# Kernel optimization log

Hardware: AMD Instinct MI355X
Metric: run time of the kernel (lower is better)

Reference implementation:

```python
import jax, jax.numpy as jnp
import numpy as np

N = 8192
E = 262144
NODE_IN = 128
EDGE_IN = 64
OUT = 128


def setup_inputs() -> dict:
    key = jax.random.key(0)
    k1, k2, k3, k4, k5 = jax.random.split(key, 5)
    x = jax.random.normal(k1, (N, NODE_IN), dtype=jnp.float32)
    edge_index = jax.random.randint(k2, (2, E), 0, N, dtype=jnp.int64)
    edge_attr = jax.random.normal(k3, (E, EDGE_IN), dtype=jnp.float32)
    W = jax.random.normal(k4, (OUT, NODE_IN), dtype=jnp.float32) / np.sqrt(NODE_IN)
    a = jax.random.normal(k5, (1, 2 * OUT + EDGE_IN), dtype=jnp.float32) / np.sqrt(2 * OUT + EDGE_IN)
    return {"x": x, "edge_index": edge_index, "edge_attr": edge_attr, "W": W, "a": a}


def reference(x, edge_index, edge_attr, W, a):
    # h = W(x): [N, out]
    h = x @ W.T
    src, dst = edge_index[0], edge_index[1]
    # per-edge concat [h_src, h_dst, edge_attr]: [E, 2*out + edge_in]
    a_input = jnp.concatenate([h[src], h[dst], edge_attr], axis=1)
    # e = leakyrelu(a(a_input)): [E]
    e = jax.nn.leaky_relu(a_input @ a.T, negative_slope=0.2).squeeze(-1)
    n = h.shape[0]
    # dense scatter into NxN (non-edges stay 0 and DO participate in softmax,
    # matching the original torch module)
    attention = jnp.zeros((n, n), dtype=x.dtype).at[src, dst].set(e)
    attention = jax.nn.softmax(attention, axis=1)
    # aggregate: [N, out]
    return attention @ h
```

## Files before the change

### kernel.cpp

```cpp
#include <hip/hip_runtime.h>

#define N_NODES 8192
#define N_EDGES 262144
#define CAP 128
#define BM 16
#define NB_GEMM 512
#define NEB2 1024
#define NSB 32

typedef float vf4 __attribute__((ext_vector_type(4)));

__device__ inline unsigned short f2bf(float f) {
    unsigned u = __float_as_uint(f);
    u += 0x7FFF + ((u >> 16) & 1);
    return (unsigned short)(u >> 16);
}

__global__ __launch_bounds__(256) void k_gemm(const float* __restrict__ x,
                                              const float* __restrict__ W,
                                              const float* __restrict__ a,
                                              unsigned short* __restrict__ h2,
                                              float* __restrict__ asrc,
                                              float* __restrict__ adst,
                                              float* __restrict__ Spart,
                                              int* __restrict__ counts) {
    __shared__ float wlds[128 * 128];
    __shared__ float xlds[BM * 128];
    __shared__ float csum_l[4 * 130];

    const int tid = threadIdx.x;
    const int tc = tid & 63;
    const int tr = tid >> 6;
    const int r0 = blockIdx.x * BM;

    if (tid < BM) counts[blockIdx.x * BM + tid] = 0;

    #pragma unroll
    for (int i = tid; i < BM * 32; i += 256) {
        const int row = i >> 5, k4 = (i & 31) << 2;
        const vf4 v = __builtin_nontemporal_load(
            reinterpret_cast<const vf4*>(&x[(size_t)(r0 + row) * 128 + k4]));
        *reinterpret_cast<vf4*>(&xlds[row * 128 + k4]) = v;
    }
    #pragma unroll
    for (int i = tid; i < 4096; i += 256) {
        const int wr = i >> 5, k4 = (i & 31) << 2;
        const int ks = k4 ^ (((wr >> 1) & 31) << 2);
        *reinterpret_cast<float4*>(&wlds[wr * 128 + ks]) =
            *reinterpret_cast<const float4*>(&W[(size_t)wr * 128 + k4]);
    }
    __syncthreads();

    float acc[4][2] = {};
    const int R0 = 2 * tc;
    const int sw = (tc & 31) << 2;
    #pragma unroll 8
    for (int k0 = 0; k0 < 128; k0 += 4) {
        const int ks = k0 ^ sw;
        const float4 w0 = *reinterpret_cast<const float4*>(&wlds[R0 * 128 + ks]);
        const float4 w1 = *reinterpret_cast<const float4*>(&wlds[(R0 + 1) * 128 + ks]);
        #pragma unroll
        for (int r = 0; r < 4; ++r) {
            const float4 xv = *reinterpret_cast<const float4*>(&xlds[(4 * tr + r) * 128 + k0]);
            acc[r][0] += xv.x*w0.x + xv.y*w0.y + xv.z*w0.z + xv.w*w0.w;
            acc[r][1] += xv.x*w1.x + xv.y*w1.y + xv.z*w1.z + xv.w*w1.w;
        }
    }

    #pragma unroll
    for (int r = 0; r < 4; ++r) {
        ushort2 o; o.x = f2bf(acc[r][0]); o.y = f2bf(acc[r][1]);
        *reinterpret_cast<ushort2*>(&h2[(size_t)(r0 + 4 * tr + r) * 128 + 2 * tc]) = o;
    }
    {
        float2 cs;
        cs.x = acc[0][0] + acc[1][0] + acc[2][0] + acc[3][0];
        cs.y = acc[0][1] + acc[1][1] + acc[2][1] + acc[3][1];
        *reinterpret_cast<float2*>(&csum_l[tr * 130 + 2 * tc]) = cs;
    }

    const float a10 = a[2*tc], a11 = a[2*tc+1];
    const float a20 = a[128+2*tc], a21 = a[128+2*tc+1];
    #pragma unroll
    for (int r = 0; r < 4; ++r) {
        float v1 = acc[r][0]*a10 + acc[r][1]*a11;
        float v2 = acc[r][0]*a20 + acc[r][1]*a21;
        #pragma unroll
        for (int o = 32; o > 0; o >>= 1) { v1 += __shfl_down(v1, o); v2 += __shfl_down(v2, o); }
        if (tc == 0) { asrc[r0 + 4*tr + r] = v1; adst[r0 + 4*tr + r] = v2; }
    }
    __syncthreads();
    if (tid < 128) {
        const float s = csum_l[tid] + csum_l[130 + tid] + csum_l[260 + tid] + csum_l[390 + tid];
        Spart[(size_t)blockIdx.x * 128 + tid] = s;
    }
}

__global__ __launch_bounds__(256) void k_edge(const int* __restrict__ ei,
                                              const float* __restrict__ ea,
                                              const float* __restrict__ a,
                                              const float* __restrict__ asrc,
                                              const float* __restrict__ adst,
                                              int* __restrict__ counts,
                                              int2* __restrict__ bucket,
                                              const float* __restrict__ Spart,
                                              float* __restrict__ S) {
    const int blk = blockIdx.x;
    const int tid = threadIdx.x;
    if (blk >= NEB2) {
        const int c = (blk - NEB2) * 4 + (tid >> 6);
        const int l = tid & 63;
        float s = 0.f;
        #pragma unroll
        for (int j = 0; j < 8; ++j) s += Spart[(size_t)(l + 64 * j) * 128 + c];
        #pragma unroll
        for (int o = 32; o > 0; o >>= 1) s += __shfl_down(s, o);
        if (l == 0) S[c] = s;
        return;
    }
    __shared__ float d_l[256];
    const int lane16 = tid & 15;
    const int grp = tid >> 4;
    const int ebase = blk * 256;
    const int eid = ebase + tid;

    const int s = __builtin_nontemporal_load(&ei[eid]);
    const int t = __builtin_nontemporal_load(&ei[N_EDGES + eid]);
    const float as_ = asrc[s];
    const float at_ = adst[t];

    const float4 av = *reinterpret_cast<const float4*>(&a[256 + lane16 * 4]);
    #pragma unroll 4
    for (int p = 0; p < 16; ++p) {
        const int e2 = ebase + p * 16 + grp;
        const vf4 ev = __builtin_nontemporal_load(
            reinterpret_cast<const vf4*>(&ea[(size_t)e2 * 64 + lane16 * 4]));
        float d = ev.x*av.x + ev.y*av.y + ev.z*av.z + ev.w*av.w;
        d += __shfl_xor(d, 1);
        d += __shfl_xor(d, 2);
        d += __shfl_xor(d, 4);
        d += __shfl_xor(d, 8);
        if (lane16 == 0) d_l[p * 16 + grp] = d;
    }
    __syncthreads();
    const float v = as_ + at_ + d_l[tid];
    const float ev = v > 0.f ? v : 0.2f * v;
    const int pos = atomicAdd(&counts[s], 1);
    if (pos < CAP) {
        int2 rec;
        rec.x = (int)(((unsigned)eid << 13) | (unsigned)t);
        rec.y = __float_as_int(ev);
        bucket[(size_t)s * CAP + pos] = rec;
    }
}

__global__ __launch_bounds__(256) void k_row(const int2* __restrict__ bucket2,
                                             const int* __restrict__ counts,
                                             const unsigned short* __restrict__ h2,
                                             const float* __restrict__ S,
                                             float* __restrict__ out) {
    __shared__ __align__(16) int key_l[2][CAP];
    __shared__ float e_l[2][CAP];
    __shared__ float cw[2][CAP];
    __shared__ int cd[2][CAP];
    __shared__ float redm[2][2], reds[2][2];
    __shared__ float4 xw[2][32];
    __shared__ int nw_s[2];

    const int tid = threadIdx.x;
    const int sub = tid >> 7;
    const int t = tid & 127;
    const int q = t & 31;
    const int g = t >> 5;
    const int row = blockIdx.x * 2 + sub;
    const float4 Sv4 = *reinterpret_cast<const float4*>(&S[4 * q]);

    const int2 rec = bucket2[(size_t)row * CAP + t];
    int k = counts[row];
    if (k > CAP) k = CAP;
    const int kpad = (k + 3) & ~3;
    if (t < k) {
        key_l[sub][t] = rec.x;
        e_l[sub][t] = __int_as_float(rec.y);
    } else if (t < kpad) {
        key_l[sub][t] = -1;
    }
    if (t == 0) nw_s[sub] = 0;
    __syncthreads();

    float mloc = 0.f;
    if (t < k) {
        const int key = key_l[sub][t];
        bool win = true;
        for (int s2 = 0; s2 < kpad; s2 += 4) {
            const int4 kv = *reinterpret_cast<const int4*>(&key_l[sub][s2]);
            const bool hit = (((kv.x ^ key) & 8191) == 0 && kv.x > key)
                          || (((kv.y ^ key) & 8191) == 0 && kv.y > key)
                          || (((kv.z ^ key) & 8191) == 0 && kv.z > key)
                          || (((kv.w ^ key) & 8191) == 0 && kv.w > key);
            win = win && !hit;
        }
        if (win) {
            const float ev = e_l[sub][t];
            mloc = ev > 0.f ? ev : 0.f;
            const int p = atomicAdd(&nw_s[sub], 1);
            cd[sub][p] = key & 8191;
            cw[sub][p] = ev;
        }
    }
    #pragma unroll
    for (int o = 32; o > 0; o >>= 1) mloc = fmaxf(mloc, __shfl_down(mloc, o));
    if ((t & 63) == 0) redm[sub][t >> 6] = mloc;
    __syncthreads();
    const float m = fmaxf(redm[sub][0], redm[sub][1]);
    const int nw = nw_s[sub];
    const float w0 = expf(-m);
    float sloc = 0.f;
    if (t < nw) {
        const float w = expf(cw[sub][t] - m);
        sloc = w;
        cw[sub][t] = w - w0;
    }
    #pragma unroll
    for (int o = 32; o > 0; o >>= 1) sloc += __shfl_down(sloc, o);
    if ((t & 63) == 0) reds[sub][t >> 6] = sloc;
    __syncthreads();
    const float D = (float)(N_NODES - nw) * w0 + reds[sub][0] + reds[sub][1];

    float4 acc0 = {0.f, 0.f, 0.f, 0.f}, acc1 = {0.f, 0.f, 0.f, 0.f};
    int j = g;
    for (; j + 4 < nw; j += 8) {
        const float c0 = cw[sub][j], c1 = cw[sub][j + 4];
        const int d0 = cd[sub][j], d1 = cd[sub][j + 4];
        const ushort4 u0 = *reinterpret_cast<const ushort4*>(&h2[(size_t)d0 * 128 + 4 * q]);
        const ushort4 u1 = *reinterpret_cast<const ushort4*>(&h2[(size_t)d1 * 128 + 4 * q]);
        acc0.x += c0 * __uint_as_float((unsigned)u0.x << 16);
        acc0.y += c0 * __uint_as_float((unsigned)u0.y << 16);
        acc0.z += c0 * __uint_as_float((unsigned)u0.z << 16);
        acc0.w += c0 * __uint_as_float((unsigned)u0.w << 16);
        acc1.x += c1 * __uint_as_float((unsigned)u1.x << 16);
        acc1.y += c1 * __uint_as_float((unsigned)u1.y << 16);
        acc1.z += c1 * __uint_as_float((unsigned)u1.z << 16);
        acc1.w += c1 * __uint_as_float((unsigned)u1.w << 16);
    }
    for (; j < nw; j += 4) {
        const float c0 = cw[sub][j];
        const ushort4 u0 = *reinterpret_cast<const ushort4*>(&h2[(size_t)cd[sub][j] * 128 + 4 * q]);
        acc0.x += c0 * __uint_as_float((unsigned)u0.x << 16);
        acc0.y += c0 * __uint_as_float((unsigned)u0.y << 16);
        acc0.z += c0 * __uint_as_float((unsigned)u0.z << 16);
        acc0.w += c0 * __uint_as_float((unsigned)u0.w << 16);
    }
    float4 acc4;
    acc4.x = acc0.x + acc1.x;
    acc4.y = acc0.y + acc1.y;
    acc4.z = acc0.z + acc1.z;
    acc4.w = acc0.w + acc1.w;
    acc4.x += __shfl_down(acc4.x, 32);
    acc4.y += __shfl_down(acc4.y, 32);
    acc4.z += __shfl_down(acc4.z, 32);
    acc4.w += __shfl_down(acc4.w, 32);
    if (t >= 64 && t < 96) xw[sub][q] = acc4;
    __syncthreads();
    if (t < 32) {
        const float4 tt = xw[sub][q];
        float4 o;
        o.x = (w0 * Sv4.x + acc4.x + tt.x) / D;
        o.y = (w0 * Sv4.y + acc4.y + tt.y) / D;
        o.z = (w0 * Sv4.z + acc4.z + tt.z) / D;
        o.w = (w0 * Sv4.w + acc4.w + tt.w) / D;
        *reinterpret_cast<float4*>(&out[(size_t)row * 128 + 4 * q]) = o;
    }
}

extern "C" void kernel_launch(void* const* d_in, const int* in_sizes, int n_in,
                              void* d_out, int out_size, void* d_ws, size_t ws_size,
                              hipStream_t stream) {
    const float* x = (const float*)d_in[0];
    const int* ei = (const int*)d_in[1];
    const float* ea = (const float*)d_in[2];
    const float* W = (const float*)d_in[3];
    const float* a = (const float*)d_in[4];
    float* out = (float*)d_out;

    char* ws = (char*)d_ws;
    unsigned short* h2 = (unsigned short*)(ws);
    int2* bucket = (int2*)(ws + (2 << 20));
    float* Spart = (float*)(ws + (10 << 20));
    float* asrc = (float*)(ws + (10 << 20) + 262144);
    float* adst = (float*)(ws + (10 << 20) + 294912);
    int* counts = (int*)(ws + (10 << 20) + 327680);
    float* S = (float*)(ws + (10 << 20) + 360448);

    k_gemm<<<NB_GEMM, 256, 0, stream>>>(x, W, a, h2, asrc, adst, Spart, counts);
    k_edge<<<NEB2 + NSB, 256, 0, stream>>>(ei, ea, a, asrc, adst, counts, bucket, Spart, S);
    k_row<<<N_NODES / 2, 256, 0, stream>>>(bucket, counts, h2, S, out);
}
```

Measured before the change: 60.23 us.

## Move edge-attribute dot products into the GEMM kernel as interleaved blocks

The edge_attr·a dot products move out of the edge kernel into extra blocks of the first kernel, interleaved one GEMM block to two edge-attr blocks, and write a per-edge scalar buffer. The edge kernel becomes a light gather-and-scatter that reads that buffer, and the row kernel now loads bucket records only for valid slots. The aim is to overlap the 64 MB edge_attr stream with the compute-bound GEMM and shorten the atomic-bound edge kernel. In exchange it adds a 1 MB intermediate write and read, and GEMM blocks that use a lot of LDS now share CUs with streaming blocks.

```diff
diff --git a/kernel.cpp b/kernel.cpp
--- a/kernel.cpp
+++ b/kernel.cpp
@@ -5,6 +5,7 @@
 #define CAP 128
 #define BM 16
 #define NB_GEMM 512
+#define NB_EA 1024
 #define NEB2 1024
 #define NSB 32
 
@@ -16,24 +17,50 @@
     return (unsigned short)(u >> 16);
 }
 
-__global__ __launch_bounds__(256) void k_gemm(const float* __restrict__ x,
-                                              const float* __restrict__ W,
-                                              const float* __restrict__ a,
-                                              unsigned short* __restrict__ h2,
-                                              float* __restrict__ asrc,
-                                              float* __restrict__ adst,
-                                              float* __restrict__ Spart,
-                                              int* __restrict__ counts) {
+__global__ __launch_bounds__(256) void k_fused1(const float* __restrict__ x,
+                                                const float* __restrict__ W,
+                                                const float* __restrict__ a,
+                                                const float* __restrict__ ea,
+                                                unsigned short* __restrict__ h2,
+                                                float* __restrict__ asrc,
+                                                float* __restrict__ adst,
+                                                float* __restrict__ Spart,
+                                                int* __restrict__ counts,
+                                                float* __restrict__ d) {
     __shared__ float wlds[128 * 128];
     __shared__ float xlds[BM * 128];
     __shared__ float csum_l[4 * 130];
 
+    const int b = blockIdx.x;
     const int tid = threadIdx.x;
+
+    if (b % 3 != 0) {
+        const int eablk = b - (b / 3) - 1;
+        const int lane16 = tid & 15;
+        const int grp = tid >> 4;
+        const int ebase = eablk * 256;
+        const float4 av = *reinterpret_cast<const float4*>(&a[256 + lane16 * 4]);
+        #pragma unroll 4
+        for (int p = 0; p < 16; ++p) {
+            const int e2 = ebase + p * 16 + grp;
+            const vf4 ev = __builtin_nontemporal_load(
+                reinterpret_cast<const vf4*>(&ea[(size_t)e2 * 64 + lane16 * 4]));
+            float dv = ev.x*av.x + ev.y*av.y + ev.z*av.z + ev.w*av.w;
+            dv += __shfl_xor(dv, 1);
+            dv += __shfl_xor(dv, 2);
+            dv += __shfl_xor(dv, 4);
+            dv += __shfl_xor(dv, 8);
+            if (lane16 == 0) d[e2] = dv;
+        }
+        return;
+    }
+
+    const int gb = b / 3;
     const int tc = tid & 63;
     const int tr = tid >> 6;
-    const int r0 = blockIdx.x * BM;
-
-    if (tid < BM) counts[blockIdx.x * BM + tid] = 0;
+    const int r0 = gb * BM;
+
+    if (tid < BM) counts[gb * BM + tid] = 0;
 
     #pragma unroll
     for (int i = tid; i < BM * 32; i += 256) {
@@ -92,13 +119,12 @@
     __syncthreads();
     if (tid < 128) {
         const float s = csum_l[tid] + csum_l[130 + tid] + csum_l[260 + tid] + csum_l[390 + tid];
-        Spart[(size_t)blockIdx.x * 128 + tid] = s;
+        Spart[(size_t)gb * 128 + tid] = s;
     }
 }
 
 __global__ __launch_bounds__(256) void k_edge(const int* __restrict__ ei,
-                                              const float* __restrict__ ea,
-                                              const float* __restrict__ a,
+                                              const float* __restrict__ d,
                                               const float* __restrict__ asrc,
                                               const float* __restrict__ adst,
                                               int* __restrict__ counts,
@@ -118,32 +144,10 @@
         if (l == 0) S[c] = s;
         return;
     }
-    __shared__ float d_l[256];
-    const int lane16 = tid & 15;
-    const int grp = tid >> 4;
-    const int ebase = blk * 256;
-    const int eid = ebase + tid;
-
+    const int eid = blk * 256 + tid;
     const int s = __builtin_nontemporal_load(&ei[eid]);
     const int t = __builtin_nontemporal_load(&ei[N_EDGES + eid]);
-    const float as_ = asrc[s];
-    const float at_ = adst[t];
-
-    const float4 av = *reinterpret_cast<const float4*>(&a[256 + lane16 * 4]);
-    #pragma unroll 4
-    for (int p = 0; p < 16; ++p) {
-        const int e2 = ebase + p * 16 + grp;
-        const vf4 ev = __builtin_nontemporal_load(
-            reinterpret_cast<const vf4*>(&ea[(size_t)e2 * 64 + lane16 * 4]));
-        float d = ev.x*av.x + ev.y*av.y + ev.z*av.z + ev.w*av.w;
-        d += __shfl_xor(d, 1);
-        d += __shfl_xor(d, 2);
-        d += __shfl_xor(d, 4);
-        d += __shfl_xor(d, 8);
-        if (lane16 == 0) d_l[p * 16 + grp] = d;
-    }
-    __syncthreads();
-    const float v = as_ + at_ + d_l[tid];
+    const float v = asrc[s] + adst[t] + d[eid];
     const float ev = v > 0.f ? v : 0.2f * v;
     const int pos = atomicAdd(&counts[s], 1);
     if (pos < CAP) {
@@ -175,11 +179,11 @@
     const int row = blockIdx.x * 2 + sub;
     const float4 Sv4 = *reinterpret_cast<const float4*>(&S[4 * q]);
 
-    const int2 rec = bucket2[(size_t)row * CAP + t];
     int k = counts[row];
     if (k > CAP) k = CAP;
     const int kpad = (k + 3) & ~3;
     if (t < k) {
+        const int2 rec = bucket2[(size_t)row * CAP + t];
         key_l[sub][t] = rec.x;
         e_l[sub][t] = __int_as_float(rec.y);
     } else if (t < kpad) {
@@ -286,13 +290,15 @@
     char* ws = (char*)d_ws;
     unsigned short* h2 = (unsigned short*)(ws);
     int2* bucket = (int2*)(ws + (2 << 20));
-    float* Spart = (float*)(ws + (10 << 20));
-    float* asrc = (float*)(ws + (10 << 20) + 262144);
-    float* adst = (float*)(ws + (10 << 20) + 294912);
-    int* counts = (int*)(ws + (10 << 20) + 327680);
-    float* S = (float*)(ws + (10 << 20) + 360448);
-
-    k_gemm<<<NB_GEMM, 256, 0, stream>>>(x, W, a, h2, asrc, adst, Spart, counts);
-    k_edge<<<NEB2 + NSB, 256, 0, stream>>>(ei, ea, a, asrc, adst, counts, bucket, Spart, S);
+    float* dbuf = (float*)(ws + (10 << 20));
+    float* Spart = (float*)(ws + (11 << 20));
+    float* asrc = (float*)(ws + (11 << 20) + 262144);
+    float* adst = (float*)(ws + (11 << 20) + 294912);
+    int* counts = (int*)(ws + (11 << 20) + 327680);
+    float* S = (float*)(ws + (11 << 20) + 360448);
+
+    k_fused1<<<NB_GEMM + NB_EA, 256, 0, stream>>>(x, W, a, ea, h2, asrc, adst,
+                                                  Spart, counts, dbuf);
+    k_edge<<<NEB2 + NSB, 256, 0, stream>>>(ei, dbuf, asrc, adst, counts, bucket, Spart, S);
     k_row<<<N_NODES / 2, 256, 0, stream>>>(bucket, counts, h2, S, out);
 }
```

After: 73.99 us. 1.23x slower.
